# Performance work log

Hardware: AMD Instinct MI355X
Metric: run time of the kernel (lower is better)

The kernel has to match this reference:

```python
import jax, jax.numpy as jnp
import numpy as np

B, L, T = 8192, 1024, 4  # batch, seq_len, n_tags (BMES)


def setup_inputs() -> dict:
    key = jax.random.key(0)
    k1, k2, k3, k4, k5 = jax.random.split(key, 5)
    return {
        "s_tag": jax.random.normal(k1, (B, L, T), dtype=jnp.float32),
        "tags": jax.random.randint(k2, (B, L), 0, T),
        "mask": jnp.ones((B, L), dtype=bool),
        "trans_score": (jax.random.normal(k3, (T, T), dtype=jnp.float32) * 0.1),
        "start_score": (jax.random.normal(k4, (T,), dtype=jnp.float32) * 0.1),
        "end_score": (jax.random.normal(k5, (T,), dtype=jnp.float32) * 0.1),
    }


def reference(s_tag, tags, mask, trans_score, start_score, end_score):
    # forward() path of LinearCRFWordSegmentation: loss = (logZ - gold_score)/B.
    # Note: forward calls set_mask(False), so the structural masks are unused.
    b, l, t = s_tag.shape
    bidx = jnp.arange(b)
    end_pos = mask.sum(axis=-1) - 1  # [B] index of last valid position

    # ---- gold path score (get_scores) ----
    emit = jnp.take_along_axis(s_tag, tags[..., None], axis=-1)[..., 0]  # [B,L]
    trans = trans_score[tags[:, :-1], tags[:, 1:]]                        # [B,L-1]
    per_pos = emit + jnp.pad(trans, ((0, 0), (1, 0)))                     # [B,L]
    score = jnp.sum(jnp.where(mask, per_pos, jnp.float32(0)))
    score = score + start_score[tags[:, 0]].sum()
    score = score + end_score[tags[bidx, end_pos]].sum()

    # ---- log partition (crf): sequential logsumexp recurrence over tags ----
    s0 = s_tag[:, 0] + start_score  # [B,T]

    def step(s_prev, emit_t):
        # [B,T_prev,1] + [1,T_prev,T_cur] + [B,1,T_cur] -> logsumexp over prev
        s_new = jax.nn.logsumexp(
            s_prev[:, :, None] + trans_score[None] + emit_t[:, None, :], axis=1
        )
        return s_new, s_new

    emits = jnp.swapaxes(s_tag, 0, 1)  # [L,B,T]
    _, ss = jax.lax.scan(step, s0, emits[1:])      # [L-1,B,T]
    ss = jnp.concatenate([s0[None], ss], axis=0)    # [L,B,T] alpha trellis
    final = ss[end_pos, bidx] + end_score           # [B,T]
    logZ = jax.nn.logsumexp(final, axis=-1).sum()

    return (logZ - score) / jnp.float32(b)
```

## Files before the change

### kernel.cpp

```cpp
#include <hip/hip_runtime.h>

#define Bn 8192
#define Ln 1024

#define LOG2E 1.4426950408889634f
#define LN2f  0.6931471805599453f

typedef float f32x2 __attribute__((ext_vector_type(2)));

__device__ __forceinline__ float sel4(float4 v, int t) {
    float r = v.x;
    r = (t == 1) ? v.y : r;
    r = (t == 2) ? v.z : r;
    r = (t == 3) ? v.w : r;
    return r;
}

__device__ __forceinline__ float rfl(float x) {
    return __int_as_float(__builtin_amdgcn_readfirstlane(__float_as_int(x)));
}

__device__ __forceinline__ float fexp2(float x) {
    float r;
    asm("v_exp_f32 %0, %1" : "=v"(r) : "v"(x));
    return r;
}

__device__ __forceinline__ f32x2 pkmax(f32x2 a, f32x2 b) {
    return (f32x2){fmaxf(a.x, b.x), fmaxf(a.y, b.y)};
}

__device__ __forceinline__ void tile8(
    const float4 st[8], const int tg[8], const float es[4][4],
    float p[4][4], int& scale, float& emitsum, bool skip0)
{
    f32x2 pc[4][2];
#pragma unroll
    for (int j = 0; j < 4; j++) {
        pc[j][0] = (f32x2){(j == 0) ? 1.f : 0.f, (j == 1) ? 1.f : 0.f};
        pc[j][1] = (f32x2){(j == 2) ? 1.f : 0.f, (j == 3) ? 1.f : 0.f};
    }

#pragma unroll
    for (int j = 0; j < 8; j++) {
        emitsum += sel4(st[j], tg[j]);
        if (!(skip0 && j == 0)) {
            float f0 = fexp2(st[j].x * LOG2E);
            float f1 = fexp2(st[j].y * LOG2E);
            float f2 = fexp2(st[j].z * LOG2E);
            float f3 = fexp2(st[j].w * LOG2E);

            f32x2 n00 = pc[0][0] * es[0][0] + pc[1][0] * es[1][0] + pc[2][0] * es[2][0] + pc[3][0] * es[3][0];
            f32x2 n01 = pc[0][1] * es[0][0] + pc[1][1] * es[1][0] + pc[2][1] * es[2][0] + pc[3][1] * es[3][0];
            f32x2 n10 = pc[0][0] * es[0][1] + pc[1][0] * es[1][1] + pc[2][0] * es[2][1] + pc[3][0] * es[3][1];
            f32x2 n11 = pc[0][1] * es[0][1] + pc[1][1] * es[1][1] + pc[2][1] * es[2][1] + pc[3][1] * es[3][1];
            f32x2 n20 = pc[0][0] * es[0][2] + pc[1][0] * es[1][2] + pc[2][0] * es[2][2] + pc[3][0] * es[3][2];
            f32x2 n21 = pc[0][1] * es[0][2] + pc[1][1] * es[1][2] + pc[2][1] * es[2][2] + pc[3][1] * es[3][2];
            f32x2 n30 = pc[0][0] * es[0][3] + pc[1][0] * es[1][3] + pc[2][0] * es[2][3] + pc[3][0] * es[3][3];
            f32x2 n31 = pc[0][1] * es[0][3] + pc[1][1] * es[1][3] + pc[2][1] * es[2][3] + pc[3][1] * es[3][3];
            pc[0][0] = n00 * f0; pc[0][1] = n01 * f0;
            pc[1][0] = n10 * f1; pc[1][1] = n11 * f1;
            pc[2][0] = n20 * f2; pc[2][1] = n21 * f2;
            pc[3][0] = n30 * f3; pc[3][1] = n31 * f3;
        }
    }
    {
        f32x2 mm = pkmax(pkmax(pkmax(pc[0][0], pc[0][1]), pkmax(pc[1][0], pc[1][1])),
                         pkmax(pkmax(pc[2][0], pc[2][1]), pkmax(pc[3][0], pc[3][1])));
        float mx = fmaxf(mm.x, mm.y);
        unsigned eb = (__float_as_uint(mx) >> 23) & 0xffu;
        scale += (int)eb - 126;
        float ms = __uint_as_float((unsigned)(253 - eb) << 23);
#pragma unroll
        for (int jj = 0; jj < 4; jj++) { pc[jj][0] *= ms; pc[jj][1] *= ms; }
    }
#pragma unroll
    for (int i = 0; i < 4; i++)
#pragma unroll
        for (int j = 0; j < 4; j++) p[i][j] = pc[j][i >> 1][i & 1];
}

__device__ __forceinline__ void butterfly3(float p[4][4], int& scale, int lw) {
#pragma unroll
    for (int s = 0; s < 3; s++) {
        const int m = 1 << s;
        float q[4][4];
#pragma unroll
        for (int i = 0; i < 4; i++)
#pragma unroll
            for (int j = 0; j < 4; j++) q[i][j] = __shfl_xor(p[i][j], m);
        int sc2 = __shfl_xor(scale, m);
        bool upper = (lw & m) != 0;
        float A[4][4], Bm[4][4];
#pragma unroll
        for (int i = 0; i < 4; i++)
#pragma unroll
            for (int j = 0; j < 4; j++) {
                A[i][j]  = upper ? q[i][j] : p[i][j];
                Bm[i][j] = upper ? p[i][j] : q[i][j];
            }
#pragma unroll
        for (int i = 0; i < 4; i++)
#pragma unroll
            for (int j = 0; j < 4; j++)
                p[i][j] = A[i][0] * Bm[0][j] + A[i][1] * Bm[1][j]
                        + A[i][2] * Bm[2][j] + A[i][3] * Bm[3][j];
        scale += sc2;

        float mx = p[0][0];
#pragma unroll
        for (int i = 0; i < 4; i++)
#pragma unroll
            for (int j = 0; j < 4; j++) mx = fmaxf(mx, p[i][j]);
        unsigned eb = (__float_as_uint(mx) >> 23) & 0xffu;
        scale += (int)eb - 126;
        float ms = __uint_as_float((unsigned)(253 - eb) << 23);
#pragma unroll
        for (int i = 0; i < 4; i++)
#pragma unroll
            for (int j = 0; j < 4; j++) p[i][j] *= ms;
    }
}

__global__ __launch_bounds__(64) void crf_half(
    const float* __restrict__ s_tag, const int* __restrict__ tags,
    const float* __restrict__ trans,
    float* __restrict__ wsP, int* __restrict__ wsK, float* __restrict__ wsS)
{
    __shared__ float4 sS[512];

    const int lw = threadIdx.x;
    const int hb = blockIdx.x;

    const float4* __restrict__ srow = (const float4*)s_tag + (size_t)hb * 512;
    const int*    __restrict__ trow = tags + (size_t)hb * 512;

    int prev_c = trow[(hb == 0) ? 0 : -1];

    const int4* trow4 = (const int4*)trow;
    int4 ta = trow4[2 * lw], tb = trow4[2 * lw + 1];

    const int swl = lw ^ ((lw >> 3) & 7);
    float4 v[8];
#pragma unroll
    for (int k = 0; k < 8; k++) v[k] = srow[64 * k + swl];

    int tg[8] = {ta.x, ta.y, ta.z, ta.w, tb.x, tb.y, tb.z, tb.w};
    const bool skip0 = (hb == 0) && (lw == 0);

    int pl = __shfl(tg[7], (lw + 63) & 63);
    int prev = (lw == 0) ? prev_c : pl;

    float vtr = trans[lw & 15];
    float trsum = 0.f;
    {
        int pt = prev;
#pragma unroll
        for (int j = 0; j < 8; j++) {
            float g = __shfl(vtr, pt * 4 + tg[j]);
            trsum += (skip0 && j == 0) ? 0.f : g;
            pt = tg[j];
        }
    }
    float es[4][4];
#pragma unroll
    for (int k = 0; k < 4; k++)
#pragma unroll
        for (int j = 0; j < 4; j++)
            es[k][j] = rfl(fexp2(trans[k * 4 + j] * LOG2E));

#pragma unroll
    for (int k = 0; k < 8; k++) sS[64 * k + lw] = v[k];

    float4 st[8];
#pragma unroll
    for (int j = 0; j < 8; j++)
        st[j] = sS[8 * lw + (j ^ (lw & 7))];

    float p[4][4];
    int scale = 0;
    float emitsum = 0.f;
    tile8(st, tg, es, p, scale, emitsum, skip0);
    butterfly3(p, scale, lw);

    float sc = emitsum + trsum;
#pragma unroll
    for (int m = 1; m < 64; m <<= 1) sc += __shfl_xor(sc, m);
    if (lw == 0) wsS[hb] = sc;

    if ((lw & 7) == 0) {
        size_t idx = (size_t)hb * 8 + (lw >> 3);
        float4* P4 = (float4*)wsP + idx * 4;
        P4[0] = make_float4(p[0][0], p[0][1], p[0][2], p[0][3]);
        P4[1] = make_float4(p[1][0], p[1][1], p[1][2], p[1][3]);
        P4[2] = make_float4(p[2][0], p[2][1], p[2][2], p[2][3]);
        P4[3] = make_float4(p[3][0], p[3][1], p[3][2], p[3][3]);
        wsK[idx] = scale;
    }
}

__global__ __launch_bounds__(256) void crf_fin(
    const float* __restrict__ s_tag, const int* __restrict__ tags,
    const float* __restrict__ start_s, const float* __restrict__ end_s,
    const float* __restrict__ wsP, const int* __restrict__ wsK,
    const float* __restrict__ wsS, float* __restrict__ diffs)
{
    const int t = threadIdx.x;
    const int sub = t & 15;
    const int b = blockIdx.x * 16 + (t >> 4);

    const float4* P4 = (const float4*)wsP + ((size_t)b * 16 + sub) * 4;
    float4 r0 = P4[0], r1 = P4[1], r2 = P4[2], r3 = P4[3];
    float p[4][4] = {{r0.x, r0.y, r0.z, r0.w}, {r1.x, r1.y, r1.z, r1.w},
                     {r2.x, r2.y, r2.z, r2.w}, {r3.x, r3.y, r3.z, r3.w}};
    int scale = wsK[(size_t)b * 16 + sub];

#pragma unroll
    for (int s = 0; s < 4; s++) {
        const int m = 1 << s;
        float q[4][4];
#pragma unroll
        for (int i = 0; i < 4; i++)
#pragma unroll
            for (int j = 0; j < 4; j++) q[i][j] = __shfl_xor(p[i][j], m);
        int sc2 = __shfl_xor(scale, m);
        bool upper = (sub & m) != 0;
        float A[4][4], Bm[4][4];
#pragma unroll
        for (int i = 0; i < 4; i++)
#pragma unroll
            for (int j = 0; j < 4; j++) {
                A[i][j]  = upper ? q[i][j] : p[i][j];
                Bm[i][j] = upper ? p[i][j] : q[i][j];
            }
#pragma unroll
        for (int i = 0; i < 4; i++)
#pragma unroll
            for (int j = 0; j < 4; j++)
                p[i][j] = A[i][0] * Bm[0][j] + A[i][1] * Bm[1][j]
                        + A[i][2] * Bm[2][j] + A[i][3] * Bm[3][j];
        scale += sc2;

        float mx = p[0][0];
#pragma unroll
        for (int i = 0; i < 4; i++)
#pragma unroll
            for (int j = 0; j < 4; j++) mx = fmaxf(mx, p[i][j]);
        unsigned eb = (__float_as_uint(mx) >> 23) & 0xffu;
        scale += (int)eb - 126;
        float ms = __uint_as_float((unsigned)(253 - eb) << 23);
#pragma unroll
        for (int i = 0; i < 4; i++)
#pragma unroll
            for (int j = 0; j < 4; j++) p[i][j] *= ms;
    }

    if (sub == 0) {
        float4 st0 = *((const float4*)s_tag + (size_t)b * Ln);
        float a0 = exp2f((st0.x + start_s[0]) * LOG2E);
        float a1 = exp2f((st0.y + start_s[1]) * LOG2E);
        float a2 = exp2f((st0.z + start_s[2]) * LOG2E);
        float a3 = exp2f((st0.w + start_s[3]) * LOG2E);

        float n0 = a0 * p[0][0] + a1 * p[1][0] + a2 * p[2][0] + a3 * p[3][0];
        float n1 = a0 * p[0][1] + a1 * p[1][1] + a2 * p[2][1] + a3 * p[3][1];
        float n2 = a0 * p[0][2] + a1 * p[1][2] + a2 * p[2][2] + a3 * p[3][2];
        float n3 = a0 * p[0][3] + a1 * p[1][3] + a2 * p[2][3] + a3 * p[3][3];

        float sfin = n0 * exp2f(end_s[0] * LOG2E) + n1 * exp2f(end_s[1] * LOG2E)
                   + n2 * exp2f(end_s[2] * LOG2E) + n3 * exp2f(end_s[3] * LOG2E);
        float logZ = (log2f(sfin) + (float)scale) * LN2f;

        int t0 = tags[(size_t)b * Ln];
        int tE = tags[(size_t)b * Ln + Ln - 1];
        float gold = wsS[(size_t)b * 2] + wsS[(size_t)b * 2 + 1]
                   + start_s[t0] + end_s[tE];
        diffs[b] = logZ - gold;
    }
}

__global__ __launch_bounds__(1024) void crf_pass3(
    const float* __restrict__ diffs, float* __restrict__ out)
{
    __shared__ float sm[1024];
    float s = 0.f;
    for (int i = threadIdx.x; i < Bn; i += 1024) s += diffs[i];
    sm[threadIdx.x] = s;
    __syncthreads();
    for (int off = 512; off > 0; off >>= 1) {
        if ((int)threadIdx.x < off) sm[threadIdx.x] += sm[threadIdx.x + off];
        __syncthreads();
    }
    if (threadIdx.x == 0) out[0] = sm[0] / (float)Bn;
}

extern "C" void kernel_launch(void* const* d_in, const int* in_sizes, int n_in,
                              void* d_out, int out_size, void* d_ws, size_t ws_size,
                              hipStream_t stream)
{
    const float* s_tag  = (const float*)d_in[0];
    const int*   tags   = (const int*)d_in[1];
    const float* trans  = (const float*)d_in[3];
    const float* starts = (const float*)d_in[4];
    const float* ends   = (const float*)d_in[5];

    float* wsP   = (float*)d_ws;
    int*   wsK   = (int*)(wsP + (size_t)Bn * 16 * 16);
    float* wsS   = (float*)(wsK + (size_t)Bn * 16);
    float* diffs = wsS + (size_t)Bn * 2;

    crf_half<<<dim3(Bn * 2), dim3(64), 0, stream>>>(
        s_tag, tags, trans, wsP, wsK, wsS);
    crf_fin<<<dim3(Bn / 16), dim3(256), 0, stream>>>(
        s_tag, tags, starts, ends, wsP, wsK, wsS, diffs);
    crf_pass3<<<dim3(1), dim3(1024), 0, stream>>>(diffs, (float*)d_out);
}
```

Baseline: 50.03 us.

## Fuse three CRF kernels into one with in-block combine and atomic final reduction

Measured after the change: 158.5 us. 217% more time.

```diff
diff --git a/kernel.cpp b/kernel.cpp
--- a/kernel.cpp
+++ b/kernel.cpp
@@ -2,9 +2,11 @@
 
 #define Bn 8192
 #define Ln 1024
+#define NBLOCK (Bn / 2)
 
 #define LOG2E 1.4426950408889634f
 #define LN2f  0.6931471805599453f
+#define ACC_SCALE 4294967296.0
 
 typedef float f32x2 __attribute__((ext_vector_type(2)));
 
@@ -80,9 +82,10 @@
         for (int j = 0; j < 4; j++) p[i][j] = pc[j][i >> 1][i & 1];
 }
 
-__device__ __forceinline__ void butterfly3(float p[4][4], int& scale, int lw) {
-#pragma unroll
-    for (int s = 0; s < 3; s++) {
+template <int LEVELS>
+__device__ __forceinline__ void butterfly(float p[4][4], int& scale, int lane) {
+#pragma unroll
+    for (int s = 0; s < LEVELS; s++) {
         const int m = 1 << s;
         float q[4][4];
 #pragma unroll
@@ -90,7 +93,7 @@
 #pragma unroll
             for (int j = 0; j < 4; j++) q[i][j] = __shfl_xor(p[i][j], m);
         int sc2 = __shfl_xor(scale, m);
-        bool upper = (lw & m) != 0;
+        bool upper = (lane & m) != 0;
         float A[4][4], Bm[4][4];
 #pragma unroll
         for (int i = 0; i < 4; i++)
@@ -122,20 +125,24 @@
     }
 }
 
-__global__ __launch_bounds__(64) void crf_half(
+__global__ __launch_bounds__(256) void crf_all(
     const float* __restrict__ s_tag, const int* __restrict__ tags,
-    const float* __restrict__ trans,
-    float* __restrict__ wsP, int* __restrict__ wsK, float* __restrict__ wsS)
+    const float* __restrict__ trans, const float* __restrict__ start_s,
+    const float* __restrict__ end_s,
+    unsigned long long* __restrict__ acc, unsigned* __restrict__ cnt,
+    float* __restrict__ out)
 {
-    __shared__ float4 sS[512];
-
-    const int lw = threadIdx.x;
-    const int hb = blockIdx.x;
+    __shared__ float4 sS[2048];
+
+    const int wv = threadIdx.x >> 6;
+    const int lw = threadIdx.x & 63;
+    const int hb = (blockIdx.x << 2) | wv;
 
     const float4* __restrict__ srow = (const float4*)s_tag + (size_t)hb * 512;
     const int*    __restrict__ trow = tags + (size_t)hb * 512;
-
-    int prev_c = trow[(hb == 0) ? 0 : -1];
+    float4* slice = &sS[wv * 512];
+
+    int prev_c = trow[(hb & 1) ? -1 : 0];
 
     const int4* trow4 = (const int4*)trow;
     int4 ta = trow4[2 * lw], tb = trow4[2 * lw + 1];
@@ -146,7 +153,7 @@
     for (int k = 0; k < 8; k++) v[k] = srow[64 * k + swl];
 
     int tg[8] = {ta.x, ta.y, ta.z, ta.w, tb.x, tb.y, tb.z, tb.w};
-    const bool skip0 = (hb == 0) && (lw == 0);
+    const bool skip0 = ((hb & 1) == 0) && (lw == 0);
 
     int pl = __shfl(tg[7], (lw + 63) & 63);
     int prev = (lw == 0) ? prev_c : pl;
@@ -170,128 +177,90 @@
             es[k][j] = rfl(fexp2(trans[k * 4 + j] * LOG2E));
 
 #pragma unroll
-    for (int k = 0; k < 8; k++) sS[64 * k + lw] = v[k];
+    for (int k = 0; k < 8; k++) slice[64 * k + lw] = v[k];
 
     float4 st[8];
 #pragma unroll
     for (int j = 0; j < 8; j++)
-        st[j] = sS[8 * lw + (j ^ (lw & 7))];
+        st[j] = slice[8 * lw + (j ^ (lw & 7))];
 
     float p[4][4];
     int scale = 0;
     float emitsum = 0.f;
     tile8(st, tg, es, p, scale, emitsum, skip0);
-    butterfly3(p, scale, lw);
+    butterfly<3>(p, scale, lw);
 
     float sc = emitsum + trsum;
 #pragma unroll
     for (int m = 1; m < 64; m <<= 1) sc += __shfl_xor(sc, m);
-    if (lw == 0) wsS[hb] = sc;
+
+    __syncthreads();
+
+    float4* exM = sS;
+    int*    exK = (int*)(sS + 128);
+    float*  exS = (float*)(sS + 136);
 
     if ((lw & 7) == 0) {
-        size_t idx = (size_t)hb * 8 + (lw >> 3);
-        float4* P4 = (float4*)wsP + idx * 4;
-        P4[0] = make_float4(p[0][0], p[0][1], p[0][2], p[0][3]);
-        P4[1] = make_float4(p[1][0], p[1][1], p[1][2], p[1][3]);
-        P4[2] = make_float4(p[2][0], p[2][1], p[2][2], p[2][3]);
-        P4[3] = make_float4(p[3][0], p[3][1], p[3][2], p[3][3]);
-        wsK[idx] = scale;
-    }
-}
-
-__global__ __launch_bounds__(256) void crf_fin(
-    const float* __restrict__ s_tag, const int* __restrict__ tags,
-    const float* __restrict__ start_s, const float* __restrict__ end_s,
-    const float* __restrict__ wsP, const int* __restrict__ wsK,
-    const float* __restrict__ wsS, float* __restrict__ diffs)
-{
-    const int t = threadIdx.x;
-    const int sub = t & 15;
-    const int b = blockIdx.x * 16 + (t >> 4);
-
-    const float4* P4 = (const float4*)wsP + ((size_t)b * 16 + sub) * 4;
-    float4 r0 = P4[0], r1 = P4[1], r2 = P4[2], r3 = P4[3];
-    float p[4][4] = {{r0.x, r0.y, r0.z, r0.w}, {r1.x, r1.y, r1.z, r1.w},
-                     {r2.x, r2.y, r2.z, r2.w}, {r3.x, r3.y, r3.z, r3.w}};
-    int scale = wsK[(size_t)b * 16 + sub];
-
-#pragma unroll
-    for (int s = 0; s < 4; s++) {
-        const int m = 1 << s;
-        float q[4][4];
-#pragma unroll
-        for (int i = 0; i < 4; i++)
-#pragma unroll
-            for (int j = 0; j < 4; j++) q[i][j] = __shfl_xor(p[i][j], m);
-        int sc2 = __shfl_xor(scale, m);
-        bool upper = (sub & m) != 0;
-        float A[4][4], Bm[4][4];
-#pragma unroll
-        for (int i = 0; i < 4; i++)
-#pragma unroll
-            for (int j = 0; j < 4; j++) {
-                A[i][j]  = upper ? q[i][j] : p[i][j];
-                Bm[i][j] = upper ? p[i][j] : q[i][j];
-            }
-#pragma unroll
-        for (int i = 0; i < 4; i++)
-#pragma unroll
-            for (int j = 0; j < 4; j++)
-                p[i][j] = A[i][0] * Bm[0][j] + A[i][1] * Bm[1][j]
-                        + A[i][2] * Bm[2][j] + A[i][3] * Bm[3][j];
-        scale += sc2;
-
-        float mx = p[0][0];
-#pragma unroll
-        for (int i = 0; i < 4; i++)
-#pragma unroll
-            for (int j = 0; j < 4; j++) mx = fmaxf(mx, p[i][j]);
-        unsigned eb = (__float_as_uint(mx) >> 23) & 0xffu;
-        scale += (int)eb - 126;
-        float ms = __uint_as_float((unsigned)(253 - eb) << 23);
-#pragma unroll
-        for (int i = 0; i < 4; i++)
-#pragma unroll
-            for (int j = 0; j < 4; j++) p[i][j] *= ms;
-    }
-
-    if (sub == 0) {
-        float4 st0 = *((const float4*)s_tag + (size_t)b * Ln);
+        int m = wv * 8 + (lw >> 3);
+        exM[m * 4 + 0] = make_float4(p[0][0], p[0][1], p[0][2], p[0][3]);
+        exM[m * 4 + 1] = make_float4(p[1][0], p[1][1], p[1][2], p[1][3]);
+        exM[m * 4 + 2] = make_float4(p[2][0], p[2][1], p[2][2], p[2][3]);
+        exM[m * 4 + 3] = make_float4(p[3][0], p[3][1], p[3][2], p[3][3]);
+        exK[m] = scale;
+    }
+    if (lw == 0) exS[wv] = sc;
+    __syncthreads();
+
+    if (threadIdx.x < 32) {
+        const int t   = threadIdx.x;
+        const int sub = t & 15;
+        const int bl  = t >> 4;
+        const long long batch = 2LL * blockIdx.x + bl;
+
+        float4 r0 = exM[(bl * 16 + sub) * 4 + 0];
+        float4 r1 = exM[(bl * 16 + sub) * 4 + 1];
+        float4 r2 = exM[(bl * 16 + sub) * 4 + 2];
+        float4 r3 = exM[(bl * 16 + sub) * 4 + 3];
+        float pf[4][4] = {{r0.x, r0.y, r0.z, r0.w}, {r1.x, r1.y, r1.z, r1.w},
+                          {r2.x, r2.y, r2.z, r2.w}, {r3.x, r3.y, r3.z, r3.w}};
+        int fsc = exK[bl * 16 + sub];
+
+        butterfly<4>(pf, fsc, sub);
+
+        float4 st0 = *((const float4*)s_tag + (size_t)batch * Ln);
         float a0 = exp2f((st0.x + start_s[0]) * LOG2E);
         float a1 = exp2f((st0.y + start_s[1]) * LOG2E);
         float a2 = exp2f((st0.z + start_s[2]) * LOG2E);
         float a3 = exp2f((st0.w + start_s[3]) * LOG2E);
 
-        float n0 = a0 * p[0][0] + a1 * p[1][0] + a2 * p[2][0] + a3 * p[3][0];
-        float n1 = a0 * p[0][1] + a1 * p[1][1] + a2 * p[2][1] + a3 * p[3][1];
-        float n2 = a0 * p[0][2] + a1 * p[1][2] + a2 * p[2][2] + a3 * p[3][2];
-        float n3 = a0 * p[0][3] + a1 * p[1][3] + a2 * p[2][3] + a3 * p[3][3];
+        float n0 = a0 * pf[0][0] + a1 * pf[1][0] + a2 * pf[2][0] + a3 * pf[3][0];
+        float n1 = a0 * pf[0][1] + a1 * pf[1][1] + a2 * pf[2][1] + a3 * pf[3][1];
+        float n2 = a0 * pf[0][2] + a1 * pf[1][2] + a2 * pf[2][2] + a3 * pf[3][2];
+        float n3 = a0 * pf[0][3] + a1 * pf[1][3] + a2 * pf[2][3] + a3 * pf[3][3];
 
         float sfin = n0 * exp2f(end_s[0] * LOG2E) + n1 * exp2f(end_s[1] * LOG2E)
                    + n2 * exp2f(end_s[2] * LOG2E) + n3 * exp2f(end_s[3] * LOG2E);
-        float logZ = (log2f(sfin) + (float)scale) * LN2f;
-
-        int t0 = tags[(size_t)b * Ln];
-        int tE = tags[(size_t)b * Ln + Ln - 1];
-        float gold = wsS[(size_t)b * 2] + wsS[(size_t)b * 2 + 1]
-                   + start_s[t0] + end_s[tE];
-        diffs[b] = logZ - gold;
-    }
-}
-
-__global__ __launch_bounds__(1024) void crf_pass3(
-    const float* __restrict__ diffs, float* __restrict__ out)
-{
-    __shared__ float sm[1024];
-    float s = 0.f;
-    for (int i = threadIdx.x; i < Bn; i += 1024) s += diffs[i];
-    sm[threadIdx.x] = s;
-    __syncthreads();
-    for (int off = 512; off > 0; off >>= 1) {
-        if ((int)threadIdx.x < off) sm[threadIdx.x] += sm[threadIdx.x + off];
-        __syncthreads();
-    }
-    if (threadIdx.x == 0) out[0] = sm[0] / (float)Bn;
+        float logZ = (log2f(sfin) + (float)fsc) * LN2f;
+
+        int t0 = tags[(size_t)batch * Ln];
+        int tE = tags[(size_t)batch * Ln + Ln - 1];
+        float gold = exS[2 * bl] + exS[2 * bl + 1] + start_s[t0] + end_s[tE];
+        float diff = logZ - gold;
+
+        float d16 = __shfl(diff, 16);
+        if (t == 0) {
+            double dsum = (double)diff + (double)d16;
+            long long contrib = (long long)(dsum * ACC_SCALE);
+            atomicAdd(acc, (unsigned long long)contrib);
+            __threadfence();
+            unsigned old = atomicAdd(cnt, 1u);
+            if (old == NBLOCK - 1) {
+                unsigned long long raw = atomicAdd(acc, 0ULL);
+                double tot = (double)(long long)raw * (1.0 / ACC_SCALE);
+                out[0] = (float)(tot / (double)Bn);
+            }
+        }
+    }
 }
 
 extern "C" void kernel_launch(void* const* d_in, const int* in_sizes, int n_in,
@@ -304,14 +273,11 @@
     const float* starts = (const float*)d_in[4];
     const float* ends   = (const float*)d_in[5];
 
-    float* wsP   = (float*)d_ws;
-    int*   wsK   = (int*)(wsP + (size_t)Bn * 16 * 16);
-    float* wsS   = (float*)(wsK + (size_t)Bn * 16);
-    float* diffs = wsS + (size_t)Bn * 2;
-
-    crf_half<<<dim3(Bn * 2), dim3(64), 0, stream>>>(
-        s_tag, tags, trans, wsP, wsK, wsS);
-    crf_fin<<<dim3(Bn / 16), dim3(256), 0, stream>>>(
-        s_tag, tags, starts, ends, wsP, wsK, wsS, diffs);
-    crf_pass3<<<dim3(1), dim3(1024), 0, stream>>>(diffs, (float*)d_out);
-}
+    unsigned long long* acc = (unsigned long long*)d_ws;
+    unsigned*           cnt = (unsigned*)(acc + 1);
+
+    hipMemsetAsync(d_ws, 0, 16, stream);
+
+    crf_all<<<dim3(NBLOCK), dim3(256), 0, stream>>>(
+        s_tag, tags, trans, starts, ends, acc, cnt, (float*)d_out);
+}
```
